# Performance work log

Measured on AMD Instinct MI355X. Metric: run time of the kernel, lower is better.

## Reference

```python
import jax, jax.numpy as jnp
import numpy as np

NUM_CAPSULE = 16
DIM_CAPSULE = 32
ROUTINGS = 3


def setup_inputs() -> dict:
    key = jax.random.key(0)
    k1, k2 = jax.random.split(key)
    B, S, D = 256, 512, 256  # batch, input_num_capsule, input_dim_capsule
    x = jax.random.normal(k1, (B, S, D), dtype=jnp.float32)
    # xavier-normal-ish init for W [input_dim_capsule, num_capsule*dim_capsule]
    O = NUM_CAPSULE * DIM_CAPSULE
    std = float(np.sqrt(2.0 / (D + O)))
    W = jax.random.normal(k2, (D, O), dtype=jnp.float32) * std
    return {"x": x, "W": W}


def _squash(v, axis=-1):
    # NOTE: faithful to source: divides by sqrt(||v||^2 + 1e-7) (unit-norm style)
    s = jnp.sum(v * v, axis=axis, keepdims=True)
    return v / jnp.sqrt(s + 1e-7)


def reference(x, W):
    B, S, D = x.shape
    # u_hat: [B, num_capsule, S, dim_capsule]
    u_hat = jnp.einsum('bsd,do->bso', x, W)
    u_hat = u_hat.reshape(B, S, NUM_CAPSULE, DIM_CAPSULE).transpose(0, 2, 1, 3)
    b = jnp.zeros((B, NUM_CAPSULE, S), dtype=u_hat.dtype)
    outputs = None
    for i in range(ROUTINGS):
        # softmax over the num_capsule axis (source permutes then softmax dim=2)
        c = jax.nn.softmax(b, axis=1)  # [B, nc, S]
        outputs = _squash(jnp.einsum('bns,bnsd->bnd', c, u_hat))  # [B, nc, dc]
        if i < ROUTINGS - 1:
            b = jnp.einsum('bnd,bnsd->bns', outputs, u_hat)
    return outputs.reshape(-1, NUM_CAPSULE * DIM_CAPSULE)
```

## Files before the change

kernel.cpp:

```cpp
#include <hip/hip_runtime.h>


#define S_ 512
#define D_ 256
#define O_ 512

typedef __attribute__((ext_vector_type(8))) short short8;
typedef __attribute__((ext_vector_type(4))) float floatx4;

__device__ __forceinline__ unsigned short f2b(float f) {
  union { float ff; unsigned int i; } v; v.ff = f;
  unsigned int u = v.i;
  return (unsigned short)((u + 0x7FFFu + ((u >> 16) & 1u)) >> 16);
}

__global__ __launch_bounds__(512, 2) void caps_kernel(
    const float* __restrict__ x, const float* __restrict__ W,
    float* __restrict__ out)
{
  __shared__ __align__(16) float bl[16 * 520];
  __shared__ __align__(16) float ytmp[16 * 260];
  __shared__ __align__(16) unsigned short zb[16 * 264];
  __shared__ __align__(16) float outp[O_];

  const int tid  = threadIdx.x;
  const int wave = tid >> 6;
  const int lane = tid & 63;
  const float* xb = x + (size_t)blockIdx.x * (S_ * D_);

  for (int it = 0; it < 3; ++it) {
    if (it == 0) {
      float a0 = 0.f, a1 = 0.f, a2 = 0.f, a3 = 0.f;
      #pragma unroll 4
      for (int r = 0; r < 64; ++r) {
        const int s = (wave << 6) + r;
        const float4 xv = *(const float4*)(xb + s * D_ + (lane << 2));
        a0 += xv.x; a1 += xv.y; a2 += xv.z; a3 += xv.w;
      }
      *(float4*)(bl + wave * 520 + (lane << 2)) = make_float4(a0, a1, a2, a3);
      __syncthreads();
      if (tid < 256) {
        float v = 0.f;
        #pragma unroll
        for (int w = 0; w < 8; ++w) v += bl[w * 520 + tid];
        v *= 0.0625f;
        #pragma unroll
        for (int n = 0; n < 16; ++n) ytmp[n * 260 + tid] = v;
      }
      __syncthreads();
    } else {
      {
        const int s = tid;
        float vv[16];
        float m = -1e30f;
        #pragma unroll
        for (int n = 0; n < 16; ++n) { vv[n] = bl[n * 520 + s]; m = fmaxf(m, vv[n]); }
        float sum = 0.f;
        #pragma unroll
        for (int n = 0; n < 16; ++n) { vv[n] = __expf(vv[n] - m); sum += vv[n]; }
        const float inv = 1.f / sum;
        #pragma unroll
        for (int n = 0; n < 16; ++n) bl[n * 520 + s] = vv[n] * inv;
      }
      __syncthreads();
      float acc[16][4];
      #pragma unroll
      for (int n = 0; n < 16; ++n) { acc[n][0]=0.f; acc[n][1]=0.f; acc[n][2]=0.f; acc[n][3]=0.f; }
      for (int g = 0; g < 16; ++g) {
        const int s0 = (wave << 6) + (g << 2);
        float cc[16][4];
        #pragma unroll
        for (int n = 0; n < 16; ++n) {
          const float4 c4 = *(const float4*)(bl + n * 520 + s0);
          cc[n][0] = c4.x; cc[n][1] = c4.y; cc[n][2] = c4.z; cc[n][3] = c4.w;
        }
        #pragma unroll
        for (int j = 0; j < 4; ++j) {
          const float4 xv = *(const float4*)(xb + (s0 + j) * D_ + (lane << 2));
          #pragma unroll
          for (int n = 0; n < 16; ++n) {
            acc[n][0] += cc[n][j] * xv.x; acc[n][1] += cc[n][j] * xv.y;
            acc[n][2] += cc[n][j] * xv.z; acc[n][3] += cc[n][j] * xv.w;
          }
        }
      }
      for (int rr = 0; rr < 8; ++rr) {
        if (wave == rr) {
          #pragma unroll
          for (int n = 0; n < 16; ++n) {
            float4* p = (float4*)(ytmp + n * 260 + (lane << 2));
            if (rr == 0) { *p = make_float4(acc[n][0], acc[n][1], acc[n][2], acc[n][3]); }
            else { float4 v = *p; v.x += acc[n][0]; v.y += acc[n][1]; v.z += acc[n][2]; v.w += acc[n][3]; *p = v; }
          }
        }
        __syncthreads();
      }
    }

    {
      const int o = tid;
      const int n = o >> 5;
      float a = 0.f;
      for (int Db = 0; Db < 32; ++Db) {
        const float4 y0 = *(const float4*)(ytmp + n * 260 + (Db << 3));
        const float4 y1 = *(const float4*)(ytmp + n * 260 + (Db << 3) + 4);
        const float* wp = W + (size_t)(Db << 3) * O_ + o;
        a += y0.x * wp[0 * O_]; a += y0.y * wp[1 * O_];
        a += y0.z * wp[2 * O_]; a += y0.w * wp[3 * O_];
        a += y1.x * wp[4 * O_]; a += y1.y * wp[5 * O_];
        a += y1.z * wp[6 * O_]; a += y1.w * wp[7 * O_];
      }
      float ss = a * a;
      #pragma unroll
      for (int off = 1; off < 32; off <<= 1) ss += __shfl_xor(ss, off, 64);
      const float v = a / sqrtf(ss + 1e-7f);
      outp[o] = v;
      if (it == 2) out[(size_t)blockIdx.x * O_ + o] = v;
    }
    __syncthreads();

    if (it < 2) {
      {
        const int obase = lane << 3;
        const int n_ln  = lane >> 2;
        float ov[8];
        #pragma unroll
        for (int j = 0; j < 8; ++j) ov[j] = outp[obase + j];
        for (int r = 0; r < 32; ++r) {
          const int Dd = (wave << 5) + r;
          const float4 w0 = *(const float4*)(W + (size_t)Dd * O_ + obase);
          const float4 w1 = *(const float4*)(W + (size_t)Dd * O_ + obase + 4);
          float a = w0.x * ov[0] + w0.y * ov[1] + w0.z * ov[2] + w0.w * ov[3]
                  + w1.x * ov[4] + w1.y * ov[5] + w1.z * ov[6] + w1.w * ov[7];
          a += __shfl_xor(a, 1, 64);
          a += __shfl_xor(a, 2, 64);
          if ((lane & 3) == 0) zb[n_ln * 264 + Dd] = f2b(a);
        }
      }
      __syncthreads();
      const int l15 = lane & 15, l4 = lane >> 4;
      for (int t = 0; t < 4; ++t) {
        const int s0 = ((wave << 2) + t) << 4;
        floatx4 C = {0.f, 0.f, 0.f, 0.f};
        #pragma unroll
        for (int k = 0; k < 8; ++k) {
          const short8 A = *(const short8*)(zb + l15 * 264 + (k << 5) + (l4 << 3));
          const float* xp = xb + (s0 + l15) * D_ + (k << 5) + (l4 << 3);
          const float4 xv0 = *(const float4*)xp;
          const float4 xv1 = *(const float4*)(xp + 4);
          short8 Bf;
          Bf[0] = (short)f2b(xv0.x); Bf[1] = (short)f2b(xv0.y);
          Bf[2] = (short)f2b(xv0.z); Bf[3] = (short)f2b(xv0.w);
          Bf[4] = (short)f2b(xv1.x); Bf[5] = (short)f2b(xv1.y);
          Bf[6] = (short)f2b(xv1.z); Bf[7] = (short)f2b(xv1.w);
          C = __builtin_amdgcn_mfma_f32_16x16x32_bf16(A, Bf, C, 0, 0, 0);
        }
        #pragma unroll
        for (int rg = 0; rg < 4; ++rg)
          bl[((l4 << 2) + rg) * 520 + s0 + l15] = C[rg];
      }
      __syncthreads();
    }
  }
}

extern "C" void kernel_launch(void* const* d_in, const int* in_sizes, int n_in,
                              void* d_out, int out_size, void* d_ws, size_t ws_size,
                              hipStream_t stream) {
  const float* x = (const float*)d_in[0];
  const float* W = (const float*)d_in[1];
  float* out = (float*)d_out;
  (void)in_sizes; (void)n_in; (void)out_size; (void)d_ws; (void)ws_size;
  caps_kernel<<<256, 512, 0, stream>>>(x, W, out);
}
```

Before: 301.3 us.

## Fuse logit MFMA and softmax into per-wave weighted-sum loop

Moves the bf16 MFMA computation of routing logits out of the end-of-iteration phase and into the weighted-sum phase. Each wave now computes logits for its own 16-row tiles, does the softmax across capsules in registers with cross-lane shuffles, and writes the coefficients to a small per-wave LDS buffer that it consumes right away. This removes the large 16x520 logit buffer, one block-wide barrier and a separate softmax pass, and cuts shared memory use. In exchange the x tile is read in both fp32 and bf16 form inside one loop, and correctness depends on the intra-wave LDS ordering enforced by the inline waitcnt.

```diff
diff --git a/kernel.cpp b/kernel.cpp
--- a/kernel.cpp
+++ b/kernel.cpp
@@ -18,14 +18,16 @@
     const float* __restrict__ x, const float* __restrict__ W,
     float* __restrict__ out)
 {
-  __shared__ __align__(16) float bl[16 * 520];
   __shared__ __align__(16) float ytmp[16 * 260];
   __shared__ __align__(16) unsigned short zb[16 * 264];
   __shared__ __align__(16) float outp[O_];
+  __shared__ __align__(16) float cbuf[8 * 256];
 
   const int tid  = threadIdx.x;
   const int wave = tid >> 6;
   const int lane = tid & 63;
+  const int l15  = lane & 15;
+  const int l4   = lane >> 4;
   const float* xb = x + (size_t)blockIdx.x * (S_ * D_);
 
   for (int it = 0; it < 3; ++it) {
@@ -37,50 +39,70 @@
         const float4 xv = *(const float4*)(xb + s * D_ + (lane << 2));
         a0 += xv.x; a1 += xv.y; a2 += xv.z; a3 += xv.w;
       }
-      *(float4*)(bl + wave * 520 + (lane << 2)) = make_float4(a0, a1, a2, a3);
+      *(float4*)(cbuf + (wave << 8) + (lane << 2)) = make_float4(a0, a1, a2, a3);
       __syncthreads();
       if (tid < 256) {
         float v = 0.f;
         #pragma unroll
-        for (int w = 0; w < 8; ++w) v += bl[w * 520 + tid];
+        for (int w = 0; w < 8; ++w) v += cbuf[(w << 8) + tid];
         v *= 0.0625f;
         #pragma unroll
         for (int n = 0; n < 16; ++n) ytmp[n * 260 + tid] = v;
       }
       __syncthreads();
     } else {
-      {
-        const int s = tid;
-        float vv[16];
-        float m = -1e30f;
-        #pragma unroll
-        for (int n = 0; n < 16; ++n) { vv[n] = bl[n * 520 + s]; m = fmaxf(m, vv[n]); }
-        float sum = 0.f;
-        #pragma unroll
-        for (int n = 0; n < 16; ++n) { vv[n] = __expf(vv[n] - m); sum += vv[n]; }
-        const float inv = 1.f / sum;
-        #pragma unroll
-        for (int n = 0; n < 16; ++n) bl[n * 520 + s] = vv[n] * inv;
-      }
-      __syncthreads();
       float acc[16][4];
       #pragma unroll
       for (int n = 0; n < 16; ++n) { acc[n][0]=0.f; acc[n][1]=0.f; acc[n][2]=0.f; acc[n][3]=0.f; }
-      for (int g = 0; g < 16; ++g) {
-        const int s0 = (wave << 6) + (g << 2);
-        float cc[16][4];
+      float* cw = cbuf + (wave << 8);
+
+      #pragma unroll 1
+      for (int t = 0; t < 4; ++t) {
+        const int s0 = (wave << 6) + (t << 4);
+        floatx4 C = {0.f, 0.f, 0.f, 0.f};
         #pragma unroll
-        for (int n = 0; n < 16; ++n) {
-          const float4 c4 = *(const float4*)(bl + n * 520 + s0);
-          cc[n][0] = c4.x; cc[n][1] = c4.y; cc[n][2] = c4.z; cc[n][3] = c4.w;
+        for (int k = 0; k < 8; ++k) {
+          const short8 A = *(const short8*)(zb + l15 * 264 + (k << 5) + (l4 << 3));
+          const float* xp = xb + (s0 + l15) * D_ + (k << 5) + (l4 << 3);
+          const float4 xv0 = *(const float4*)xp;
+          const float4 xv1 = *(const float4*)(xp + 4);
+          short8 Bf;
+          Bf[0] = (short)f2b(xv0.x); Bf[1] = (short)f2b(xv0.y);
+          Bf[2] = (short)f2b(xv0.z); Bf[3] = (short)f2b(xv0.w);
+          Bf[4] = (short)f2b(xv1.x); Bf[5] = (short)f2b(xv1.y);
+          Bf[6] = (short)f2b(xv1.z); Bf[7] = (short)f2b(xv1.w);
+          C = __builtin_amdgcn_mfma_f32_16x16x32_bf16(A, Bf, C, 0, 0, 0);
         }
-        #pragma unroll
-        for (int j = 0; j < 4; ++j) {
-          const float4 xv = *(const float4*)(xb + (s0 + j) * D_ + (lane << 2));
+        float m = fmaxf(fmaxf(C[0], C[1]), fmaxf(C[2], C[3]));
+        m = fmaxf(m, __shfl_xor(m, 16, 64));
+        m = fmaxf(m, __shfl_xor(m, 32, 64));
+        const float e0 = __expf(C[0] - m), e1 = __expf(C[1] - m);
+        const float e2 = __expf(C[2] - m), e3 = __expf(C[3] - m);
+        float sm = e0 + e1 + e2 + e3;
+        sm += __shfl_xor(sm, 16, 64);
+        sm += __shfl_xor(sm, 32, 64);
+        const float inv = 1.f / sm;
+        const int nb = l4 << 2;
+        cw[(nb + 0) * 16 + l15] = e0 * inv;
+        cw[(nb + 1) * 16 + l15] = e1 * inv;
+        cw[(nb + 2) * 16 + l15] = e2 * inv;
+        cw[(nb + 3) * 16 + l15] = e3 * inv;
+        asm volatile("s_waitcnt lgkmcnt(0)" ::: "memory");
+        for (int g = 0; g < 4; ++g) {
+          float cc[16][4];
           #pragma unroll
           for (int n = 0; n < 16; ++n) {
-            acc[n][0] += cc[n][j] * xv.x; acc[n][1] += cc[n][j] * xv.y;
-            acc[n][2] += cc[n][j] * xv.z; acc[n][3] += cc[n][j] * xv.w;
+            const float4 c4 = *(const float4*)(cw + n * 16 + (g << 2));
+            cc[n][0] = c4.x; cc[n][1] = c4.y; cc[n][2] = c4.z; cc[n][3] = c4.w;
+          }
+          #pragma unroll
+          for (int j = 0; j < 4; ++j) {
+            const float4 xv = *(const float4*)(xb + (s0 + (g << 2) + j) * D_ + (lane << 2));
+            #pragma unroll
+            for (int n = 0; n < 16; ++n) {
+              acc[n][0] += cc[n][j] * xv.x; acc[n][1] += cc[n][j] * xv.y;
+              acc[n][2] += cc[n][j] * xv.z; acc[n][3] += cc[n][j] * xv.w;
+            }
           }
         }
       }
@@ -138,28 +160,6 @@
         }
       }
       __syncthreads();
-      const int l15 = lane & 15, l4 = lane >> 4;
-      for (int t = 0; t < 4; ++t) {
-        const int s0 = ((wave << 2) + t) << 4;
-        floatx4 C = {0.f, 0.f, 0.f, 0.f};
-        #pragma unroll
-        for (int k = 0; k < 8; ++k) {
-          const short8 A = *(const short8*)(zb + l15 * 264 + (k << 5) + (l4 << 3));
-          const float* xp = xb + (s0 + l15) * D_ + (k << 5) + (l4 << 3);
-          const float4 xv0 = *(const float4*)xp;
-          const float4 xv1 = *(const float4*)(xp + 4);
-          short8 Bf;
-          Bf[0] = (short)f2b(xv0.x); Bf[1] = (short)f2b(xv0.y);
-          Bf[2] = (short)f2b(xv0.z); Bf[3] = (short)f2b(xv0.w);
-          Bf[4] = (short)f2b(xv1.x); Bf[5] = (short)f2b(xv1.y);
-          Bf[6] = (short)f2b(xv1.z); Bf[7] = (short)f2b(xv1.w);
-          C = __builtin_amdgcn_mfma_f32_16x16x32_bf16(A, Bf, C, 0, 0, 0);
-        }
-        #pragma unroll
-        for (int rg = 0; rg < 4; ++rg)
-          bl[((l4 << 2) + rg) * 520 + s0 + l15] = C[rg];
-      }
-      __syncthreads();
     }
   }
 }
```

After: 285.9 us. 1.05x faster.
